# Optimization experiments

Hardware: AMD Instinct MI355X
Metric: run time of the kernel (lower is better)

The kernel has to match this reference:

```python
import jax, jax.numpy as jnp
import numpy as np

WS = 14   # window_size
NH = 12   # num_heads

def _rel_index(ws):
    # Deterministic relative-position index buffer, identical to the torch module.
    coords = np.stack(np.meshgrid(np.arange(ws), np.arange(ws), indexing='ij'))  # [2,ws,ws]
    cf = coords.reshape(2, -1)                                                   # [2,N]
    rel = (cf[:, :, None] - cf[:, None, :]).transpose(1, 2, 0).astype(np.int64)  # [N,N,2]
    rel[..., 0] += ws - 1
    rel[..., 1] += ws - 1
    rel[..., 0] *= 2 * ws - 1
    return rel.sum(-1)  # [N,N]


def setup_inputs() -> dict:
    key = jax.random.key(0)
    ks = jax.random.split(key, 5)
    B, H, W, C = 16, 56, 56, 768
    x = jax.random.normal(ks[0], (B, H * W, C), jnp.float32)
    qkv_w = jax.random.normal(ks[1], (3 * C, C), jnp.float32) * 0.02
    q_bias = jnp.zeros((C,), jnp.float32)
    v_bias = jnp.zeros((C,), jnp.float32)
    rel_bias_table = jax.random.normal(ks[2], ((2 * WS - 1) ** 2, NH), jnp.float32) * 0.02
    proj_w = jax.random.normal(ks[3], (C, C), jnp.float32) * 0.02
    proj_b = jnp.zeros((C,), jnp.float32)
    return {"x": x, "qkv_w": qkv_w, "q_bias": q_bias, "v_bias": v_bias,
            "rel_bias_table": rel_bias_table, "proj_w": proj_w, "proj_b": proj_b,
            "H": H, "W": W}


def reference(x, qkv_w, q_bias, v_bias, rel_bias_table, proj_w, proj_b, H, W):
    B, L, C = x.shape
    ws, nh = WS, NH
    hd = C // nh
    scale = hd ** (-0.5)
    N = ws * ws

    # --- window partition with pad (H_, W_ are Python ints -> static) ---
    xs = x.reshape(B, H, W, C)
    H_ = -(-H // ws) * ws
    W_ = -(-W // ws) * ws
    xs = jnp.pad(xs, ((0, 0), (0, H_ - H), (0, W_ - W), (0, 0)))
    xw = xs.reshape(B, H_ // ws, ws, W_ // ws, ws, C).transpose(0, 1, 3, 2, 4, 5)
    xw = xw.reshape(-1, N, C)  # [Bw, N, C]

    # --- qkv with q/v bias (k bias is zero) ---
    qkv_b = jnp.concatenate([q_bias, jnp.zeros_like(v_bias), v_bias])
    qkv = (xw @ qkv_w.T + qkv_b).reshape(-1, N, 3, nh, hd).transpose(2, 0, 3, 1, 4)
    q, k, v = qkv[0] * scale, qkv[1], qkv[2]  # each [Bw, nh, N, hd]

    # --- scores + gathered relative-position bias + softmax ---
    attn = jnp.einsum('bhnd,bhmd->bhnm', q, k)
    idx = jnp.asarray(_rel_index(ws).reshape(-1))
    rpb = rel_bias_table[idx].reshape(N, N, nh).transpose(2, 0, 1)  # [nh,N,N]
    attn = jax.nn.softmax(attn + rpb[None], axis=-1)

    out = jnp.einsum('bhnm,bhmd->bhnd', attn, v).transpose(0, 2, 1, 3).reshape(-1, N, C)
    out = out @ proj_w.T + proj_b

    # --- window reverse + crop ---
    out = out.reshape(B, H_ // ws, W_ // ws, ws, ws, C).transpose(0, 1, 3, 2, 4, 5)
    out = out.reshape(B, H_, W_, C)[:, :H, :W, :].reshape(B, H * W, C)
    return out
```

## Files before the change

### kernel.cpp

```cpp
#include <hip/hip_runtime.h>

typedef unsigned short u16;
typedef unsigned int   u32;
typedef __bf16  bf16x8 __attribute__((ext_vector_type(8)));
typedef float   f32x4  __attribute__((ext_vector_type(4)));
typedef u16     u16x8  __attribute__((ext_vector_type(8)));
typedef u16     u16x4  __attribute__((ext_vector_type(4)));

__device__ __forceinline__ float bf2f(u16 v) {
    union { u32 i; float f; } u; u.i = (u32)v << 16; return u.f;
}
__device__ __forceinline__ u16 f2bf(float f) {
    union { float f; u32 i; } u; u.f = f;
    u32 r = (u.i + 0x7FFFu + ((u.i >> 16) & 1u)) >> 16;
    return (u16)r;
}
__device__ __forceinline__ bf16x8 ld8(const u16* p) {
    return __builtin_bit_cast(bf16x8, *(const u16x8*)p);
}
__device__ __forceinline__ void gload16(const void* g, void* l) {
    __builtin_amdgcn_global_load_lds((__attribute__((address_space(1))) void*)g,
                                     (__attribute__((address_space(3))) void*)l, 16, 0, 0);
}

__global__ void detect_kernel(const u16* __restrict__ x, int* __restrict__ flag) {
    if (threadIdx.x == 0 && blockIdx.x == 0) {
        int plausible = 0;
        for (int j = 0; j < 64; j++) {
            float a = fabsf(bf2f(x[2 * j]));
            if (a >= 0.0009765625f && a <= 16.0f) plausible++;
        }
        *flag = (plausible >= 32) ? 0 : 1;
    }
}

__global__ __launch_bounds__(256) void convert_kernel(
    const void* __restrict__ src, u16* __restrict__ dst, int n,
    const int* __restrict__ flag)
{
    int fp32 = *flag;
    int stride = gridDim.x * 256 * 4;
    for (int i = (blockIdx.x * 256 + threadIdx.x) * 4; i < n; i += stride) {
        if (fp32) {
            float4 v = *(const float4*)((const float*)src + i);
            u16x4 o = { f2bf(v.x), f2bf(v.y), f2bf(v.z), f2bf(v.w) };
            *(u16x4*)(dst + i) = o;
        } else {
            *(u16x4*)(dst + i) = *(const u16x4*)((const u16*)src + i);
        }
    }
}

__global__ __launch_bounds__(256) void rpb_prep(const u16* __restrict__ table,
                                                u16* __restrict__ RPB) {
    int idx = blockIdx.x * 256 + threadIdx.x;
    if (idx >= 12 * 13 * 13 * 256) return;
    int r  = idx & 15;
    int c  = (idx >> 4) & 15;
    int q  = idx >> 8;
    int tn = q % 13;
    int q2 = q / 13;
    int tm = q2 % 13;
    int h  = q2 / 13;
    int m = tm * 16 + r, n = tn * 16 + c;
    float val;
    if (n >= 196) {
        val = -30000.0f;
    } else {
        int mc = m > 195 ? 195 : m;
        int i1 = mc / 14, j1 = mc % 14, i2 = n / 14, j2 = n % 14;
        int t = (i1 - i2 + 13) * 27 + (j1 - j2 + 13);
        val = bf2f(table[t * 12 + h]);
    }
    RPB[idx] = f2bf(val);
}

template <int MODE, int NCOLS>
__global__ __launch_bounds__(256) void gemm_kernel(
    const u16* __restrict__ A, const u16* __restrict__ Bw,
    const u16* __restrict__ bias0, const u16* __restrict__ bias1,
    void* __restrict__ Cc, const int* __restrict__ flag)
{
    __shared__ __align__(16) u16 As[128][32];
    __shared__ __align__(16) u16 Bs[128][32];
    __shared__ __align__(16) u16 rb[4][64][72];

    const int tid  = threadIdx.x;
    const int wave = tid >> 6, lane = tid & 63;
    const int quad = lane >> 4, l16 = lane & 15;
    const int bm = blockIdx.y * 128, bn = blockIdx.x * 128;
    const int wm = (wave >> 1) * 64, wn = (wave & 1) * 64;

    const int sr = wave * 32 + (lane >> 2);
    const int sk = (lane & 3) * 8;

    const u16* ga = A  + (size_t)(bm + sr) * 768 + sk;
    const u16* gb = Bw + (size_t)(bn + sr) * 768 + sk;
    u16* lA0 = &As[wave * 32][0];
    u16* lA1 = &As[wave * 32 + 16][0];
    u16* lB0 = &Bs[wave * 32][0];
    u16* lB1 = &Bs[wave * 32 + 16][0];

    f32x4 acc[4][4] = {};

    for (int k0 = 0; k0 < 768; k0 += 32) {
        __syncthreads();
        gload16(ga + k0,            lA0);
        gload16(ga + k0 + 16 * 768, lA1);
        gload16(gb + k0,            lB0);
        gload16(gb + k0 + 16 * 768, lB1);
        __syncthreads();
        bf16x8 af[4], bfr[4];
#pragma unroll
        for (int i = 0; i < 4; i++) af[i]  = ld8(&As[wm + i * 16 + l16][quad * 8]);
#pragma unroll
        for (int i = 0; i < 4; i++) bfr[i] = ld8(&Bs[wn + i * 16 + l16][quad * 8]);
#pragma unroll
        for (int mi = 0; mi < 4; mi++)
#pragma unroll
            for (int ni = 0; ni < 4; ni++)
                acc[mi][ni] = __builtin_amdgcn_mfma_f32_16x16x32_bf16(
                    af[mi], bfr[ni], acc[mi][ni], 0, 0, 0);
    }

    float bs[4], scl[4];
#pragma unroll
    for (int ni = 0; ni < 4; ni++) {
        int col = bn + wn + ni * 16 + l16;
        if (MODE == 0) {
            if (col < 768)       { bs[ni] = bf2f(bias0[col]);        scl[ni] = 0.125f; }
            else if (col < 1536) { bs[ni] = 0.f;                     scl[ni] = 1.f; }
            else                 { bs[ni] = bf2f(bias1[col - 1536]); scl[ni] = 1.f; }
        } else {
            bs[ni] = bf2f(bias0[col]); scl[ni] = 1.f;
        }
    }
#pragma unroll
    for (int mi = 0; mi < 4; mi++)
#pragma unroll
        for (int ni = 0; ni < 4; ni++)
#pragma unroll
            for (int r = 0; r < 4; r++)
                rb[wave][mi * 16 + quad * 4 + r][ni * 16 + l16] =
                    f2bf((acc[mi][ni][r] + bs[ni]) * scl[ni]);
    __asm__ volatile("s_waitcnt lgkmcnt(0)" ::: "memory");

    const int fp32out = (MODE == 1) ? *flag : 0;
#pragma unroll
    for (int i = 0; i < 8; i++) {
        int row = i * 8 + (lane >> 3);
        int cg  = (lane & 7) * 8;
        u16x8 val = *(const u16x8*)&rb[wave][row][cg];
        int gm = bm + wm + row;
        int gn = bn + wn + cg;
        size_t off;
        if (MODE == 0) {
            off = (size_t)gm * NCOLS + gn;
        } else {
            int wwin = gm / 196, t = gm % 196;
            int b2 = wwin >> 4, wh2 = (wwin >> 2) & 3, ww2 = wwin & 3;
            int ti = t / 14, tj = t % 14;
            int g = b2 * 3136 + (wh2 * 14 + ti) * 56 + ww2 * 14 + tj;
            off = (size_t)g * NCOLS + gn;
        }
        if (MODE == 1 && fp32out) {
            float* outf = (float*)Cc;
            float4 lo = { bf2f(val[0]), bf2f(val[1]), bf2f(val[2]), bf2f(val[3]) };
            float4 hi = { bf2f(val[4]), bf2f(val[5]), bf2f(val[6]), bf2f(val[7]) };
            *(float4*)&outf[off]     = lo;
            *(float4*)&outf[off + 4] = hi;
        } else {
            *(u16x8*)&((u16*)Cc)[off] = val;
        }
    }
}

__global__ __launch_bounds__(256) void attn_kernel(
    const u16* __restrict__ QKV, const u16* __restrict__ RPB, u16* __restrict__ O)
{
    __shared__ __align__(16) u16 k_s[208][72];
    __shared__ __align__(16) u16 v_t[64][224];
    __shared__ __align__(16) u16 p_s[4][16][40];

    const int tid  = threadIdx.x;
    const int wave = tid >> 6, lane = tid & 63;
    const int quad = lane >> 4, l16 = lane & 15;
    const int w = blockIdx.x / 12, h = blockIdx.x % 12;
    const int b = w >> 4, wh = (w >> 2) & 3, ww = w & 3;
    const int gbase = b * 3136 + wh * 14 * 56 + ww * 14;

    for (int c = tid; c < 1568; c += 256) {
        int tok = c >> 3, dg = c & 7;
        int ti = tok / 14, tj = tok % 14;
        size_t grow = (size_t)(gbase + ti * 56 + tj) * 2304 + h * 64 + dg * 8;
        uint4 kk = *(const uint4*)&QKV[grow + 768];
        *(uint4*)&k_s[tok][dg * 8] = kk;
        uint4 vv = *(const uint4*)&QKV[grow + 1536];
        const u16* pv = (const u16*)&vv;
#pragma unroll
        for (int j = 0; j < 8; j++) v_t[dg * 8 + j][tok] = pv[j];
    }
    for (int c = tid; c < 12 * 64; c += 256) k_s[196 + (c >> 6)][c & 63] = 0;
    for (int c = tid; c < 64 * 28; c += 256) v_t[c / 28][196 + c % 28] = 0;
    __syncthreads();

    for (int tm = wave; tm < 13; tm += 4) {
        int tq = tm * 16 + l16; if (tq > 195) tq = 195;
        int qi = tq / 14, qj = tq % 14;
        size_t qoff = (size_t)(gbase + qi * 56 + qj) * 2304 + h * 64 + quad * 8;
        bf16x8 aq0 = ld8(&QKV[qoff]);
        bf16x8 aq1 = ld8(&QKV[qoff + 32]);

        f32x4 sc[13];
#pragma unroll
        for (int tn = 0; tn < 13; tn++) {
            bf16x8 bk0 = ld8(&k_s[tn * 16 + l16][quad * 8]);
            bf16x8 bk1 = ld8(&k_s[tn * 16 + l16][32 + quad * 8]);
            f32x4 z = {};
            z = __builtin_amdgcn_mfma_f32_16x16x32_bf16(aq0, bk0, z, 0, 0, 0);
            sc[tn] = __builtin_amdgcn_mfma_f32_16x16x32_bf16(aq1, bk1, z, 0, 0, 0);
        }
#pragma unroll
        for (int tn = 0; tn < 13; tn++) {
            const u16* rp = &RPB[((((h * 13 + tm) * 13 + tn) * 16 + l16) << 4) + quad * 4];
#pragma unroll
            for (int r = 0; r < 4; r++) sc[tn][r] += bf2f(rp[r]);
        }
        float inv[4];
#pragma unroll
        for (int r = 0; r < 4; r++) {
            float m = -3.0e38f;
#pragma unroll
            for (int tn = 0; tn < 13; tn++) m = fmaxf(m, sc[tn][r]);
#pragma unroll
            for (int d = 1; d < 16; d <<= 1) m = fmaxf(m, __shfl_xor(m, d, 64));
            float s = 0.f;
#pragma unroll
            for (int tn = 0; tn < 13; tn++) {
                float e = __expf(sc[tn][r] - m);
                sc[tn][r] = e; s += e;
            }
#pragma unroll
            for (int d = 1; d < 16; d <<= 1) s += __shfl_xor(s, d, 64);
            inv[r] = 1.f / s;
        }
        f32x4 oc[4] = {};
#pragma unroll
        for (int s7 = 0; s7 < 7; s7++) {
#pragma unroll
            for (int tt = 0; tt < 2; tt++) {
                int tn = 2 * s7 + tt;
#pragma unroll
                for (int r = 0; r < 4; r++) {
                    float pv = (tn < 13) ? sc[tn][r] * inv[r] : 0.f;
                    p_s[wave][quad * 4 + r][tt * 16 + l16] = f2bf(pv);
                }
            }
            __asm__ volatile("s_waitcnt lgkmcnt(0)" ::: "memory");
            bf16x8 ap = ld8(&p_s[wave][l16][quad * 8]);
#pragma unroll
            for (int dt = 0; dt < 4; dt++) {
                bf16x8 bv = ld8(&v_t[dt * 16 + l16][s7 * 32 + quad * 8]);
                oc[dt] = __builtin_amdgcn_mfma_f32_16x16x32_bf16(ap, bv, oc[dt], 0, 0, 0);
            }
        }
#pragma unroll
        for (int dt = 0; dt < 4; dt++)
#pragma unroll
            for (int r = 0; r < 4; r++) {
                int t = tm * 16 + quad * 4 + r;
                if (t < 196)
                    O[(size_t)(w * 196 + t) * 768 + h * 64 + dt * 16 + l16] = f2bf(oc[dt][r]);
            }
    }
}

extern "C" void kernel_launch(void* const* d_in, const int* in_sizes, int n_in,
                              void* d_out, int out_size, void* d_ws, size_t ws_size,
                              hipStream_t stream) {
    char* ws = (char*)d_ws;
    u16* qkv     = (u16*)(ws);
    u16* xbf     = (u16*)(ws + 231211008);
    u16* attnout = xbf;
    u16* wqkv_bf = (u16*)(ws + 308281344);
    u16* wproj_bf= (u16*)(ws + 311820288);
    u16* rpb     = (u16*)(ws + 312999936);
    u16* qb_bf   = (u16*)(ws + 314038272);
    u16* vb_bf   = (u16*)(ws + 314039808);
    u16* pb_bf   = (u16*)(ws + 314041344);
    u16* tbl_bf  = (u16*)(ws + 314042880);
    int* flag    = (int*)(ws + 314060384);

    detect_kernel<<<1, 64, 0, stream>>>((const u16*)d_in[0], flag);
    convert_kernel<<<4096, 256, 0, stream>>>(d_in[0], xbf,      16 * 3136 * 768, flag);
    convert_kernel<<<1728, 256, 0, stream>>>(d_in[1], wqkv_bf,  2304 * 768,      flag);
    convert_kernel<<< 576, 256, 0, stream>>>(d_in[5], wproj_bf, 768 * 768,       flag);
    convert_kernel<<<   1, 256, 0, stream>>>(d_in[2], qb_bf,    768,             flag);
    convert_kernel<<<   1, 256, 0, stream>>>(d_in[3], vb_bf,    768,             flag);
    convert_kernel<<<   1, 256, 0, stream>>>(d_in[6], pb_bf,    768,             flag);
    convert_kernel<<<   9, 256, 0, stream>>>(d_in[4], tbl_bf,   729 * 12,        flag);

    rpb_prep<<<2028, 256, 0, stream>>>(tbl_bf, rpb);
    gemm_kernel<0, 2304><<<dim3(18, 392), 256, 0, stream>>>(
        xbf, wqkv_bf, qb_bf, vb_bf, qkv, flag);
    attn_kernel<<<3072, 256, 0, stream>>>(qkv, rpb, attnout);
    gemm_kernel<1, 768><<<dim3(6, 392), 256, 0, stream>>>(
        attnout, wproj_bf, pb_bf, pb_bf, d_out, flag);
}
```

Before: 800.6 us.

## Rewrite GEMM with 256x256 tiles, 4-stage LDS pipeline and XCD-aware block mapping

Replaces the 128x128 single-buffered GEMM with a 512-thread 256x256 tile kernel. It uses a 4-deep ring of async global-to-LDS loads with vmcnt waits, XOR-swizzled LDS layout to avoid bank conflicts, split A/B prefetch interleaved with MFMA, s_setprio around MFMA bursts, and a remapped 1D grid that groups consecutive tiles per XCD for L2 reuse. The aim is to hide global memory latency and raise MFMA utilization. It uses the full 128KB LDS, which limits occupancy, and M must divide 256 (50176 does).

```diff
diff --git a/kernel.cpp b/kernel.cpp
--- a/kernel.cpp
+++ b/kernel.cpp
@@ -76,101 +76,147 @@
 }
 
 template <int MODE, int NCOLS>
-__global__ __launch_bounds__(256) void gemm_kernel(
+__global__ __launch_bounds__(512, 2) void gemm_kernel(
     const u16* __restrict__ A, const u16* __restrict__ Bw,
     const u16* __restrict__ bias0, const u16* __restrict__ bias1,
     void* __restrict__ Cc, const int* __restrict__ flag)
 {
-    __shared__ __align__(16) u16 As[128][32];
-    __shared__ __align__(16) u16 Bs[128][32];
-    __shared__ __align__(16) u16 rb[4][64][72];
+    __shared__ __align__(16) u16 lds[65536];
 
     const int tid  = threadIdx.x;
     const int wave = tid >> 6, lane = tid & 63;
     const int quad = lane >> 4, l16 = lane & 15;
-    const int bm = blockIdx.y * 128, bn = blockIdx.x * 128;
-    const int wm = (wave >> 1) * 64, wn = (wave & 1) * 64;
-
-    const int sr = wave * 32 + (lane >> 2);
-    const int sk = (lane & 3) * 8;
-
-    const u16* ga = A  + (size_t)(bm + sr) * 768 + sk;
-    const u16* gb = Bw + (size_t)(bn + sr) * 768 + sk;
-    u16* lA0 = &As[wave * 32][0];
-    u16* lA1 = &As[wave * 32 + 16][0];
-    u16* lB0 = &Bs[wave * 32][0];
-    u16* lB1 = &Bs[wave * 32 + 16][0];
-
-    f32x4 acc[4][4] = {};
-
-    for (int k0 = 0; k0 < 768; k0 += 32) {
-        __syncthreads();
-        gload16(ga + k0,            lA0);
-        gload16(ga + k0 + 16 * 768, lA1);
-        gload16(gb + k0,            lB0);
-        gload16(gb + k0 + 16 * 768, lB1);
-        __syncthreads();
-        bf16x8 af[4], bfr[4];
-#pragma unroll
-        for (int i = 0; i < 4; i++) af[i]  = ld8(&As[wm + i * 16 + l16][quad * 8]);
-#pragma unroll
-        for (int i = 0; i < 4; i++) bfr[i] = ld8(&Bs[wn + i * 16 + l16][quad * 8]);
-#pragma unroll
-        for (int mi = 0; mi < 4; mi++)
-#pragma unroll
-            for (int ni = 0; ni < 4; ni++)
-                acc[mi][ni] = __builtin_amdgcn_mfma_f32_16x16x32_bf16(
-                    af[mi], bfr[ni], acc[mi][ni], 0, 0, 0);
-    }
+    const int wr = wave >> 2, wc = wave & 3;
+
+    const int nwg = gridDim.x;
+    const int qq = nwg >> 3, rr = nwg & 7;
+    const int xcd = blockIdx.x & 7, sub = blockIdx.x >> 3;
+    const int wgid = (xcd < rr ? xcd * (qq + 1)
+                               : rr * (qq + 1) + (xcd - rr) * qq) + sub;
+    const int NT  = NCOLS / 256;
+    const int bmt = wgid / NT;
+    const int bnt = wgid - bmt * NT;
+    const int bm  = bmt * 256, bn = bnt * 256;
+
+    const int uA0 = tid, uA1 = tid + 512;
+    const int rA0 = uA0 >> 2, rA1 = uA1 >> 2;
+    const int cA0 = (uA0 & 3) ^ ((uA0 >> 3) & 3);
+    const int cA1 = (uA1 & 3) ^ ((uA1 >> 3) & 3);
+    const u16* gA0 = A  + (size_t)(bm + rA0) * 768 + cA0 * 8;
+    const u16* gA1 = A  + (size_t)(bm + rA1) * 768 + cA1 * 8;
+    const u16* gB0 = Bw + (size_t)(bn + rA0) * 768 + cA0 * 8;
+    const u16* gB1 = Bw + (size_t)(bn + rA1) * 768 + cA1 * 8;
+    char* ldsb = (char*)lds;
+
+    const int cp   = quad ^ ((l16 >> 1) & 3);
+    const int offA = ((wr * 128 + l16) * 4 + cp) * 8;
+    const int offB = ((wc *  64 + l16) * 4 + cp) * 8 + 32768;
+
+#define STAGE_A(tt, ss) do {                                                  \
+    char* b_ = ldsb + (ss) * 16384 + wave * 1024;                             \
+    gload16(gA0 + (tt) * 32, b_);                                             \
+    gload16(gA1 + (tt) * 32, b_ + 8192); } while (0)
+#define STAGE_B(tt, ss) do {                                                  \
+    char* b_ = ldsb + 65536 + (ss) * 16384 + wave * 1024;                     \
+    gload16(gB0 + (tt) * 32, b_);                                             \
+    gload16(gB1 + (tt) * 32, b_ + 8192); } while (0)
+
+    STAGE_A(0, 0); STAGE_B(0, 0);
+    STAGE_A(1, 1); STAGE_B(1, 1);
+    STAGE_A(2, 2); STAGE_B(2, 2);
+
+    f32x4 acc[8][4] = {};
+    bf16x8 afr[4], bfr[4];
+
+#define TILE(t, VMC, DOSTAGE) do {                                            \
+    asm volatile("s_waitcnt vmcnt(" #VMC ")" ::: "memory");                   \
+    __builtin_amdgcn_s_barrier();                                             \
+    asm volatile("" ::: "memory");                                            \
+    const u16* sa = lds + ((t) & 3) * 8192;                                   \
+    _Pragma("unroll") for (int n = 0; n < 4; n++)                             \
+        bfr[n] = ld8(sa + offB + n * 512);                                    \
+    _Pragma("unroll") for (int m = 0; m < 4; m++)                             \
+        afr[m] = ld8(sa + offA + m * 512);                                    \
+    if (DOSTAGE) STAGE_A((t) + 3, ((t) + 3) & 3);                             \
+    __builtin_amdgcn_s_setprio(1);                                            \
+    _Pragma("unroll") for (int m = 0; m < 4; m++)                             \
+      _Pragma("unroll") for (int n = 0; n < 4; n++)                           \
+        acc[m][n] = __builtin_amdgcn_mfma_f32_16x16x32_bf16(                  \
+            afr[m], bfr[n], acc[m][n], 0, 0, 0);                              \
+    __builtin_amdgcn_s_setprio(0);                                            \
+    __builtin_amdgcn_s_barrier();                                             \
+    _Pragma("unroll") for (int m = 0; m < 4; m++)                             \
+        afr[m] = ld8(sa + offA + (m + 4) * 512);                              \
+    if (DOSTAGE) STAGE_B((t) + 3, ((t) + 3) & 3);                             \
+    __builtin_amdgcn_s_setprio(1);                                            \
+    _Pragma("unroll") for (int m = 0; m < 4; m++)                             \
+      _Pragma("unroll") for (int n = 0; n < 4; n++)                           \
+        acc[m + 4][n] = __builtin_amdgcn_mfma_f32_16x16x32_bf16(              \
+            afr[m], bfr[n], acc[m + 4][n], 0, 0, 0);                          \
+    __builtin_amdgcn_s_setprio(0);                                            \
+} while (0)
+
+    for (int t = 0; t < 21; ++t) TILE(t, 8, 1);
+    TILE(21, 8, 0);
+    TILE(22, 4, 0);
+    TILE(23, 0, 0);
+
+#undef TILE
+#undef STAGE_A
+#undef STAGE_B
+
+    __syncthreads();
 
     float bs[4], scl[4];
 #pragma unroll
-    for (int ni = 0; ni < 4; ni++) {
-        int col = bn + wn + ni * 16 + l16;
+    for (int n = 0; n < 4; n++) {
+        int col = bn + wc * 64 + n * 16 + l16;
         if (MODE == 0) {
-            if (col < 768)       { bs[ni] = bf2f(bias0[col]);        scl[ni] = 0.125f; }
-            else if (col < 1536) { bs[ni] = 0.f;                     scl[ni] = 1.f; }
-            else                 { bs[ni] = bf2f(bias1[col - 1536]); scl[ni] = 1.f; }
+            if (col < 768)       { bs[n] = bf2f(bias0[col]);        scl[n] = 0.125f; }
+            else if (col < 1536) { bs[n] = 0.f;                     scl[n] = 1.f; }
+            else                 { bs[n] = bf2f(bias1[col - 1536]); scl[n] = 1.f; }
         } else {
-            bs[ni] = bf2f(bias0[col]); scl[ni] = 1.f;
-        }
-    }
-#pragma unroll
-    for (int mi = 0; mi < 4; mi++)
-#pragma unroll
-        for (int ni = 0; ni < 4; ni++)
-#pragma unroll
-            for (int r = 0; r < 4; r++)
-                rb[wave][mi * 16 + quad * 4 + r][ni * 16 + l16] =
-                    f2bf((acc[mi][ni][r] + bs[ni]) * scl[ni]);
-    __asm__ volatile("s_waitcnt lgkmcnt(0)" ::: "memory");
-
+            bs[n] = bf2f(bias0[col]); scl[n] = 1.f;
+        }
+    }
     const int fp32out = (MODE == 1) ? *flag : 0;
-#pragma unroll
-    for (int i = 0; i < 8; i++) {
-        int row = i * 8 + (lane >> 3);
-        int cg  = (lane & 7) * 8;
-        u16x8 val = *(const u16x8*)&rb[wave][row][cg];
-        int gm = bm + wm + row;
-        int gn = bn + wn + cg;
-        size_t off;
-        if (MODE == 0) {
-            off = (size_t)gm * NCOLS + gn;
-        } else {
-            int wwin = gm / 196, t = gm % 196;
-            int b2 = wwin >> 4, wh2 = (wwin >> 2) & 3, ww2 = wwin & 3;
-            int ti = t / 14, tj = t % 14;
-            int g = b2 * 3136 + (wh2 * 14 + ti) * 56 + ww2 * 14 + tj;
-            off = (size_t)g * NCOLS + gn;
-        }
-        if (MODE == 1 && fp32out) {
-            float* outf = (float*)Cc;
-            float4 lo = { bf2f(val[0]), bf2f(val[1]), bf2f(val[2]), bf2f(val[3]) };
-            float4 hi = { bf2f(val[4]), bf2f(val[5]), bf2f(val[6]), bf2f(val[7]) };
-            *(float4*)&outf[off]     = lo;
-            *(float4*)&outf[off + 4] = hi;
-        } else {
-            *(u16x8*)&((u16*)Cc)[off] = val;
+    u16* scratch = &lds[wave * 2048];
+
+#pragma unroll
+    for (int m = 0; m < 8; m++) {
+#pragma unroll
+        for (int n = 0; n < 4; n++)
+#pragma unroll
+            for (int r2 = 0; r2 < 4; r2++)
+                scratch[(quad * 4 + r2) * 72 + n * 16 + l16] =
+                    f2bf((acc[m][n][r2] + bs[n]) * scl[n]);
+        asm volatile("s_waitcnt lgkmcnt(0)" ::: "memory");
+#pragma unroll
+        for (int j = 0; j < 2; j++) {
+            int unit = j * 64 + lane;
+            int row = unit >> 3, c8 = unit & 7;
+            u16x8 val = *(const u16x8*)&scratch[row * 72 + c8 * 8];
+            int gm = bm + wr * 128 + m * 16 + row;
+            int gn = bn + wc * 64 + c8 * 8;
+            size_t off;
+            if (MODE == 0) {
+                off = (size_t)gm * NCOLS + gn;
+            } else {
+                int wwin = gm / 196, tt = gm % 196;
+                int b2 = wwin >> 4, wh2 = (wwin >> 2) & 3, ww2 = wwin & 3;
+                int ti = tt / 14, tj = tt % 14;
+                int g = b2 * 3136 + (wh2 * 14 + ti) * 56 + ww2 * 14 + tj;
+                off = (size_t)g * NCOLS + gn;
+            }
+            if (MODE == 1 && fp32out) {
+                float* outf = (float*)Cc;
+                float4 lo = { bf2f(val[0]), bf2f(val[1]), bf2f(val[2]), bf2f(val[3]) };
+                float4 hi = { bf2f(val[4]), bf2f(val[5]), bf2f(val[6]), bf2f(val[7]) };
+                *(float4*)&outf[off]     = lo;
+                *(float4*)&outf[off + 4] = hi;
+            } else {
+                *(u16x8*)&((u16*)Cc)[off] = val;
+            }
         }
     }
 }
@@ -301,9 +347,9 @@
     convert_kernel<<<   9, 256, 0, stream>>>(d_in[4], tbl_bf,   729 * 12,        flag);
 
     rpb_prep<<<2028, 256, 0, stream>>>(tbl_bf, rpb);
-    gemm_kernel<0, 2304><<<dim3(18, 392), 256, 0, stream>>>(
+    gemm_kernel<0, 2304><<<dim3(1764), 512, 0, stream>>>(
         xbf, wqkv_bf, qb_bf, vb_bf, qkv, flag);
     attn_kernel<<<3072, 256, 0, stream>>>(qkv, rpb, attnout);
-    gemm_kernel<1, 768><<<dim3(6, 392), 256, 0, stream>>>(
+    gemm_kernel<1, 768><<<dim3(588), 512, 0, stream>>>(
         attnout, wproj_bf, pb_bf, pb_bf, d_out, flag);
 }
```

New measurement: 712.2 us. -11.0%, faster.
